# Optimization experiments

Hardware: AMD Instinct MI355X
Metric: run time of the kernel (lower is better)

The kernel has to match this reference:

```python
import jax, jax.numpy as jnp
import numpy as np

H = 64           # hidden_dim
ITERS = 24       # iterations
B, NV, NC, K = 16, 400, 440, 12   # graphs, vars/graph, clauses/graph, literals/clause
NPG = 2 * NV + NC                 # nodes per graph (2*NV literals then NC clauses)
N = B * NPG                       # total nodes = 19840


def setup_inputs() -> dict:
    rng = np.random.RandomState(0)
    key = jax.random.key(0)
    ks = iter(jax.random.split(key, 40))

    # mask: 0 for literal nodes, 1 for clause nodes
    mask_g = np.concatenate([np.zeros(2 * NV), np.ones(NC)]).astype(np.float32)
    mask = jnp.asarray(np.tile(mask_g, B))

    # flip permutation: per graph swap positive/negative literal halves, clauses identity
    perm_g = np.concatenate([np.arange(NV, 2 * NV), np.arange(NV), np.arange(2 * NV, NPG)])
    flip_perm = jnp.asarray((perm_g[None, :] + (np.arange(B) * NPG)[:, None]).ravel().astype(np.int32))

    # bipartite literal<->clause edges, both directions; self-loops added in reference
    off = (np.arange(B) * NPG)[:, None, None]
    lits = rng.randint(0, 2 * NV, size=(B, NC, K)) + off
    cls = np.broadcast_to((np.arange(NC) + 2 * NV)[None, :, None] + off, (B, NC, K))
    src = np.concatenate([lits.ravel(), cls.ravel()])
    dst = np.concatenate([cls.ravel(), lits.ravel()])
    edge_index = jnp.asarray(np.stack([src, dst]).astype(np.int32))

    def lin(i, o):
        return jax.random.normal(next(ks), (i, o), jnp.float32) / np.sqrt(i)

    def bias(o):
        return jax.random.normal(next(ks), (o,), jnp.float32) * 0.01

    x = jax.random.normal(next(ks), (N, 2), jnp.float32)
    return dict(
        x=x, mask=mask, edge_index=edge_index, flip_perm=flip_perm,
        li_w=lin(2, H), li_b=bias(H), ci_w=lin(2, H), ci_b=bias(H),
        lm1_w=lin(H, H), lm1_b=bias(H), lm2_w=lin(H, H), lm2_b=bias(H), lm3_w=lin(H, H), lm3_b=bias(H),
        cm1_w=lin(H, H), cm1_b=bias(H), cm2_w=lin(H, H), cm2_b=bias(H), cm3_w=lin(H, H), cm3_b=bias(H),
        lu_wih=lin(2 * H, 4 * H), lu_whh=lin(H, 4 * H), lu_bih=bias(4 * H), lu_bhh=bias(4 * H),
        cu_wih=lin(H, 4 * H), cu_whh=lin(H, 4 * H), cu_bih=bias(4 * H), cu_bhh=bias(4 * H),
        lv1_w=lin(H, H), lv1_b=bias(H), lv2_w=lin(H, H), lv2_b=bias(H), lv3_w=lin(H, 1), lv3_b=bias(1),
    )


def _mlp(h, w1, b1, w2, b2, w3, b3):
    # original MLP is three chained Linear layers with NO nonlinearity
    return ((h @ w1 + b1) @ w2 + b2) @ w3 + b3


def _lstm_cell(inp, h, c, wih, whh, bih, bhh):
    g = inp @ wih + h @ whh + bih + bhh          # [N, 4H], torch gate order i,f,g,o
    i, f, gg, o = jnp.split(g, 4, axis=-1)
    c2 = jax.nn.sigmoid(f) * c + jax.nn.sigmoid(i) * jnp.tanh(gg)
    h2 = jax.nn.sigmoid(o) * jnp.tanh(c2)
    return h2, c2


def _forward(x, mask, edge_index, flip_perm, params):
    (li_w, li_b, ci_w, ci_b,
     lm1_w, lm1_b, lm2_w, lm2_b, lm3_w, lm3_b,
     cm1_w, cm1_b, cm2_w, cm2_b, cm3_w, cm3_b,
     lu_wih, lu_whh, lu_bih, lu_bhh,
     cu_wih, cu_whh, cu_bih, cu_bhh,
     lv1_w, lv1_b, lv2_w, lv2_b, lv3_w, lv3_b) = params

    n = x.shape[0]
    sl = jnp.arange(n, dtype=edge_index.dtype)   # add_self_loops
    src = jnp.concatenate([edge_index[0], sl])
    dst = jnp.concatenate([edge_index[1], sl])
    m = mask[:, None]                            # [N,1]

    def prop(msgs):  # scatter-add aggregation: out[i] = sum_{(j->i)} msgs[j]
        return jax.ops.segment_sum(msgs[src], dst, num_segments=n)

    out = (x @ li_w + li_b) * (1 - m) + (x @ ci_w + ci_b) * m
    z = jnp.zeros_like(out)

    def step(carry, _):
        out, ch, cc, lh, lc = carry
        l_msg = prop(_mlp(out, lm1_w, lm1_b, lm2_w, lm2_b, lm3_w, lm3_b))
        ch, cc = _lstm_cell(l_msg, ch, cc, cu_wih, cu_whh, cu_bih, cu_bhh)
        temp = out * (1 - m) + ch * m
        c_msg = prop(_mlp(temp, cm1_w, cm1_b, cm2_w, cm2_b, cm3_w, cm3_b))
        c_in = jnp.concatenate([out[flip_perm], c_msg], axis=-1)  # flip via precomputed perm
        lh, lc = _lstm_cell(c_in, lh, lc, lu_wih, lu_whh, lu_bih, lu_bhh)
        out = lh * (1 - m) + ch * m
        return (out, ch, cc, lh, lc), None

    (out, _, _, _, _), _ = jax.lax.scan(step, (out, z, z, z, z), None, length=ITERS - 1)
    vote = _mlp(out * (1 - m), lv1_w, lv1_b, lv2_w, lv2_b, lv3_w, lv3_b)  # [N,1]
    return vote * (1 - m)


def reference(x, mask, edge_index, flip_perm,
              li_w, li_b, ci_w, ci_b,
              lm1_w, lm1_b, lm2_w, lm2_b, lm3_w, lm3_b,
              cm1_w, cm1_b, cm2_w, cm2_b, cm3_w, cm3_b,
              lu_wih, lu_whh, lu_bih, lu_bhh,
              cu_wih, cu_whh, cu_bih, cu_bhh,
              lv1_w, lv1_b, lv2_w, lv2_b, lv3_w, lv3_b):
    params = (li_w, li_b, ci_w, ci_b,
              lm1_w, lm1_b, lm2_w, lm2_b, lm3_w, lm3_b,
              cm1_w, cm1_b, cm2_w, cm2_b, cm3_w, cm3_b,
              lu_wih, lu_whh, lu_bih, lu_bhh,
              cu_wih, cu_whh, cu_bih, cu_bhh,
              lv1_w, lv1_b, lv2_w, lv2_b, lv3_w, lv3_b)
    return _forward(x, mask, edge_index, flip_perm, params)
```

## Files before the change

### kernel.cpp

```cpp
#include <hip/hip_runtime.h>
#include <math.h>


#define NV2_   800
#define NC_    440
#define KK_    12
#define NPG_   1240
#define NLIT_  12800
#define NCLS_  7040
#define NE_    84480
#define NN_    19840
#define STEPS_ 23

__device__ __forceinline__ float sigmf(float x) { return 1.0f / (1.0f + __expf(-x)); }
__device__ __forceinline__ float tanhf_(float x) { return 1.0f - 2.0f / (__expf(2.0f * x) + 1.0f); }


__global__ __launch_bounds__(64) void collapseT_k(
    const float* lm1, const float* lm1b, const float* lm2, const float* lm2b,
    const float* cm1, const float* cm1b, const float* cm2, const float* cm2b,
    float* T, float* ub)
{
    int r = blockIdx.x >> 6, i = blockIdx.x & 63, j = threadIdx.x;
    const float* w1 = r ? cm1 : lm1; const float* b1 = r ? cm1b : lm1b;
    const float* w2 = r ? cm2 : lm2; const float* b2 = r ? cm2b : lm2b;
    float s = 0.f;
    for (int k = 0; k < 64; ++k) s += w1[i * 64 + k] * w2[k * 64 + j];
    T[r * 4096 + i * 64 + j] = s;
    if (i == 0) {
        float s2 = 0.f;
        for (int k = 0; k < 64; ++k) s2 += b1[k] * w2[k * 64 + j];
        ub[r * 64 + j] = s2 + b2[j];
    }
}

__global__ __launch_bounds__(64) void collapseW_k(
    const float* lm3, const float* lm3b, const float* cm3, const float* cm3b,
    const float* T, const float* ub,
    float* Wl, float* bl, float* Wc, float* bc,
    const float* lv1, const float* lv1b, const float* lv2, const float* lv2b,
    const float* lv3, const float* lv3b, float* Wv, float* bv)
{
    int t = threadIdx.x;
    if (blockIdx.x < 128) {
        int r = blockIdx.x >> 6, i = blockIdx.x & 63, j = t;
        const float* w3 = r ? cm3 : lm3; const float* b3 = r ? cm3b : lm3b;
        float* W = r ? Wc : Wl; float* bb = r ? bc : bl;
        float s = 0.f;
        for (int k = 0; k < 64; ++k) s += T[r * 4096 + i * 64 + k] * w3[k * 64 + j];
        W[i * 64 + j] = s;
        if (i == 0) {
            float s2 = 0.f;
            for (int k = 0; k < 64; ++k) s2 += ub[r * 64 + k] * w3[k * 64 + j];
            bb[j] = s2 + b3[j];
        }
    } else {
        __shared__ float t3[64];
        __shared__ float ub2[64];
        float s = 0.f;
        for (int j = 0; j < 64; ++j) s += lv2[t * 64 + j] * lv3[j];
        t3[t] = s;
        float s2 = 0.f;
        for (int k = 0; k < 64; ++k) s2 += lv1b[k] * lv2[k * 64 + t];
        ub2[t] = s2 + lv2b[t];
        __syncthreads();
        float s3 = 0.f;
        for (int k = 0; k < 64; ++k) s3 += lv1[t * 64 + k] * t3[k];
        Wv[t] = s3;
        if (t == 0) {
            float v = 0.f;
            for (int j = 0; j < 64; ++j) v += ub2[j] * lv3[j];
            bv[0] = v + lv3b[0];
        }
    }
}

__global__ __launch_bounds__(256) void fold2_k(
    const float* Wl, const float* bl, const float* Wc, const float* bc,
    const float* lwih, const float* lbih, const float* lbhh,
    const float* cwih, const float* cbih, const float* cbhh,
    float* Wfl, float* bfl, float* Bl, float* Wfc, float* Bc)
{
    int t = blockIdx.x >> 6, i = blockIdx.x & 63, j = threadIdx.x;
    if (t == 0) {
        float s = 0.f;
        for (int m = 0; m < 64; ++m) s += Wc[i * 64 + m] * lwih[(64 + m) * 256 + j];
        Wfl[i * 256 + j] = s;
        if (i == 0) {
            float s2 = 0.f;
            for (int m = 0; m < 64; ++m) s2 += bc[m] * lwih[(64 + m) * 256 + j];
            bfl[j] = s2;
            Bl[j] = lbih[j] + lbhh[j];
        }
    } else {
        float s = 0.f;
        for (int m = 0; m < 64; ++m) s += Wl[i * 64 + m] * cwih[m * 256 + j];
        Wfc[i * 256 + j] = s;
        if (i == 0) {
            float s2 = 0.f;
            for (int m = 0; m < 64; ++m) s2 += bl[m] * cwih[m * 256 + j];
            Bc[j] = cbih[j] + cbhh[j] + 13.f * s2;
        }
    }
}

struct WT5 { const float* src[5]; float* dst[5]; };
__global__ __launch_bounds__(1024) void wtransAll_k(WT5 a)
{
    int m = blockIdx.x >> 4;
    int hc = blockIdx.x & 15;
    int half = hc >> 3, chunk = hc & 7;
    int t = threadIdx.x;
    int k = t >> 4, u4 = (t >> 2) & 3, g = t & 3;
    a.dst[m][(hc * 64 + k) * 16 + u4 * 4 + g] =
        a.src[m][k * 256 + g * 64 + half * 32 + chunk * 4 + u4];
}

__global__ __launch_bounds__(256) void init_k(
    const float* x, const float* liw, const float* lib, const float* ciw, const float* cib,
    float* out0, float* outc, float* chA, float* chB)
{
    int t = blockIdx.x * 256 + threadIdx.x;
    if (t < 64) {
        chA[(size_t)NCLS_ * 64 + t] = 0.f;
        chB[(size_t)NCLS_ * 64 + t] = 0.f;
    }
    if (t >= NN_ * 64) return;
    int node = t >> 6, j = t & 63;
    int b = node / NPG_;
    int i = node - b * NPG_;
    float x0 = x[node * 2 + 0], x1 = x[node * 2 + 1];
    if (i < NV2_) {
        int sp = (i < 400) ? 2 * i : 2 * (i - 400) + 1;
        out0[(size_t)(b * NV2_ + sp) * 64 + j] = x0 * liw[j] + x1 * liw[64 + j] + lib[j];
    } else {
        outc[(size_t)(b * NC_ + (i - NV2_)) * 64 + j] = x0 * ciw[j] + x1 * ciw[64 + j] + cib[j];
    }
}

__global__ __launch_bounds__(256) void econv_k(const int* ei, int* llits, int* cnt)
{
    int e = blockIdx.x * 256 + threadIdx.x;
    if (e >= NE_) return;
    int g = ei[e];
    int b = g / NPG_;
    int i = g - b * NPG_;
    int sp = (i < 400) ? 2 * i : 2 * (i - 400) + 1;
    int L = b * NV2_ + sp;
    llits[e] = L;
    atomicAdd(cnt + L, 1);
}

__global__ __launch_bounds__(1024) void scan_k(const int* cnt, int* rowptr, int* cursor)
{
    __shared__ int sums[1024];
    int t = threadIdx.x;
    int i0 = t * 13;
    int i1 = i0 + 13; if (i1 > NLIT_) i1 = NLIT_; if (i0 > NLIT_) i0 = NLIT_;
    int s = 0;
    for (int i = i0; i < i1; ++i) s += (cnt[i] + 7) & ~7;
    sums[t] = s;
    __syncthreads();
    for (int off = 1; off < 1024; off <<= 1) {
        int v = (t >= off) ? sums[t - off] : 0;
        __syncthreads();
        sums[t] += v;
        __syncthreads();
    }
    int run = sums[t] - s;
    for (int i = i0; i < i1; ++i) {
        rowptr[i] = run; cursor[i] = run;
        run += (cnt[i] + 7) & ~7;
    }
    if (t == 1023) rowptr[NLIT_] = sums[1023];
}

__global__ __launch_bounds__(256) void fill_k(const int* llits, int* cursor, int* col)
{
    int e = blockIdx.x * 256 + threadIdx.x;
    if (e >= NE_) return;
    int pos = atomicAdd(cursor + llits[e], 1);
    col[pos] = e / KK_;
}

__global__ __launch_bounds__(256) void pad_k(const int* cnt, const int* rowptr, int* col)
{
    int i = blockIdx.x * 256 + threadIdx.x;
    if (i >= NLIT_) return;
    for (int e = rowptr[i] + cnt[i]; e < rowptr[i + 1]; ++e) col[e] = NCLS_;
}


#define FMA16(rv, a,b,c,d) \
    acc[0]  = fmaf(rv, a.x, acc[0]);  acc[1]  = fmaf(rv, a.y, acc[1]);  \
    acc[2]  = fmaf(rv, a.z, acc[2]);  acc[3]  = fmaf(rv, a.w, acc[3]);  \
    acc[4]  = fmaf(rv, b.x, acc[4]);  acc[5]  = fmaf(rv, b.y, acc[5]);  \
    acc[6]  = fmaf(rv, b.z, acc[6]);  acc[7]  = fmaf(rv, b.w, acc[7]);  \
    acc[8]  = fmaf(rv, c.x, acc[8]);  acc[9]  = fmaf(rv, c.y, acc[9]);  \
    acc[10] = fmaf(rv, c.z, acc[10]); acc[11] = fmaf(rv, c.w, acc[11]); \
    acc[12] = fmaf(rv, d.x, acc[12]); acc[13] = fmaf(rv, d.y, acc[13]); \
    acc[14] = fmaf(rv, d.z, acc[14]); acc[15] = fmaf(rv, d.w, acc[15]);

__device__ __forceinline__ void gemmV(const float* __restrict__ Ls, int rx,
                                      const float* __restrict__ wb, float* acc)
{
    const int r = (threadIdx.x & 63) ^ rx;
    const float4* __restrict__ wp = (const float4*)wb;
#pragma unroll 4
    for (int k = 0; k < 64; ++k) {
        float4 w0 = wp[k * 4 + 0];
        float4 w1 = wp[k * 4 + 1];
        float4 w2 = wp[k * 4 + 2];
        float4 w3 = wp[k * 4 + 3];
        float rf = Ls[k * 65 + r];
        FMA16(rf, w0, w1, w2, w3);
    }
}

__device__ __forceinline__ void cellu(const float* a, float* c, float* h)
{
    float iv = sigmf(a[0]);
    float fv = sigmf(a[1]);
    float gv = tanhf_(a[2]);
    float ov = sigmf(a[3]);
    float c2 = fv * (*c) + iv * gv;
    *c = c2;
    *h = ov * tanhf_(c2);
}


__global__ __launch_bounds__(512, 4) void clause_step_k(
    const float* __restrict__ out_cur, const float* __restrict__ outc0,
    float* __restrict__ ch_cur, const float* __restrict__ ch_prev, float* __restrict__ ccg,
    const int* __restrict__ llits,
    const float* __restrict__ wfcT, const float* __restrict__ cwhhT,
    const float* __restrict__ Bc, int step)
{
    __shared__ float bufT[65 * 64];
    __shared__ float chT[65 * 64];
    const int tid = threadIdx.x;
    const int lane = tid & 63;
    const int wv = tid >> 6;
    const int half = blockIdx.x & 1;
    const int Cb = (blockIdx.x >> 1) * 64;
    const int chunk = __builtin_amdgcn_readfirstlane(wv);
    const int hc = half * 8 + chunk;

    for (int i = 0; i < 8; ++i) {
        int srow = wv * 8 + i;
        int c = Cb + srow;
        float v;
        if (step) {
            float ch0 = ch_prev[(size_t)c * 64 + lane];
            chT[lane * 65 + srow] = ch0;
            v = ch0;
        } else {
            v = outc0[(size_t)c * 64 + lane];
        }
        const int* lp = llits + c * KK_;
        float t0 = out_cur[(size_t)lp[0] * 64 + lane];
        float t1 = out_cur[(size_t)lp[1] * 64 + lane];
        float t2 = out_cur[(size_t)lp[2] * 64 + lane];
        float t3 = out_cur[(size_t)lp[3] * 64 + lane];
        float t4 = out_cur[(size_t)lp[4] * 64 + lane];
        float t5 = out_cur[(size_t)lp[5] * 64 + lane];
        float t6 = out_cur[(size_t)lp[6] * 64 + lane];
        float t7 = out_cur[(size_t)lp[7] * 64 + lane];
        float t8 = out_cur[(size_t)lp[8] * 64 + lane];
        float t9 = out_cur[(size_t)lp[9] * 64 + lane];
        float ta = out_cur[(size_t)lp[10] * 64 + lane];
        float tb = out_cur[(size_t)lp[11] * 64 + lane];
        v += t0 + t1 + t2 + t3 + t4 + t5 + t6 + t7 + t8 + t9 + ta + tb;
        bufT[lane * 65 + srow] = v;
    }
    __syncthreads();

    float acc[16];
    if (step) {
#pragma unroll
        for (int i = 0; i < 16; ++i) acc[i] = 0.f;
        gemmV(chT, 0, cwhhT + hc * 1024, acc);
#pragma unroll
        for (int u4 = 0; u4 < 4; ++u4)
#pragma unroll
            for (int g = 0; g < 4; ++g)
                acc[u4 * 4 + g] += Bc[g * 64 + half * 32 + chunk * 4 + u4];
    } else {
#pragma unroll
        for (int u4 = 0; u4 < 4; ++u4)
#pragma unroll
            for (int g = 0; g < 4; ++g)
                acc[u4 * 4 + g] = Bc[g * 64 + half * 32 + chunk * 4 + u4];
    }
    gemmV(bufT, 0, wfcT + hc * 1024, acc);

    const size_t rowbase = (size_t)(Cb + lane) * 64 + half * 32 + chunk * 4;
    float cc4[4], h4[4];
    if (step) {
        float4 cp = *(const float4*)(ccg + rowbase);
        cc4[0] = cp.x; cc4[1] = cp.y; cc4[2] = cp.z; cc4[3] = cp.w;
    } else { cc4[0] = cc4[1] = cc4[2] = cc4[3] = 0.f; }
#pragma unroll
    for (int u4 = 0; u4 < 4; ++u4) cellu(acc + u4 * 4, &cc4[u4], &h4[u4]);

    __syncthreads();
#pragma unroll
    for (int u4 = 0; u4 < 4; ++u4) {
        chT[lane * 33 + chunk * 4 + u4]  = h4[u4];
        bufT[lane * 33 + chunk * 4 + u4] = cc4[u4];
    }
    __syncthreads();
    {
        int row = tid >> 5, cl = tid & 31;
#pragma unroll
        for (int p = 0; p < 4; ++p) {
            int rr = row + p * 16;
            size_t dst = (size_t)(Cb + rr) * 64 + half * 32 + cl;
            ch_cur[dst] = chT[rr * 33 + cl];
            ccg[dst]    = bufT[rr * 33 + cl];
        }
    }
}

__global__ __launch_bounds__(512, 4) void lit_step_k(
    const float* __restrict__ out_cur, float* __restrict__ out_nxt,
    const float* __restrict__ chg, float* __restrict__ lcg,
    const int* __restrict__ rowptr, const int* __restrict__ col, const int* __restrict__ cnt,
    const float* __restrict__ wihT, const float* __restrict__ whhT, const float* __restrict__ wflT,
    const float* __restrict__ bfl, const float* __restrict__ Bl,
    const float* __restrict__ Wv, const float* __restrict__ bv, float* __restrict__ vout,
    int step)
{
    __shared__ float bufT[65 * 64 + 1024];
    const int tid = threadIdx.x;
    const int lane = tid & 63;
    const int wv = tid >> 6;
    const int half = blockIdx.x & 1;
    const int Lb = (blockIdx.x >> 1) * 64;
    const int chunk = __builtin_amdgcn_readfirstlane(wv);
    const int hc = half * 8 + chunk;

    for (int i = 0; i < 8; ++i) {
        int srow = wv * 8 + i;
        bufT[lane * 65 + srow] = out_cur[(size_t)(Lb + srow) * 64 + lane];
    }
    __syncthreads();

    const float degf = 1.f + (float)cnt[Lb + lane];
    float acc[16];
#pragma unroll
    for (int u4 = 0; u4 < 4; ++u4)
#pragma unroll
        for (int g = 0; g < 4; ++g) {
            int gc = g * 64 + half * 32 + chunk * 4 + u4;
            acc[u4 * 4 + g] = Bl[gc] + degf * bfl[gc];
        }
    gemmV(bufT, 1, wihT + hc * 1024, acc);
    if (step) gemmV(bufT, 0, whhT + hc * 1024, acc);
    __syncthreads();

    for (int i = 0; i < 8; ++i) {
        int srow = wv * 8 + i;
        int l = Lb + srow;
        int e = rowptr[l], eE = rowptr[l + 1];
        float v = bufT[lane * 65 + srow];
        for (; e < eE; e += 8) {
            float t0 = chg[(size_t)col[e    ] * 64 + lane];
            float t1 = chg[(size_t)col[e + 1] * 64 + lane];
            float t2 = chg[(size_t)col[e + 2] * 64 + lane];
            float t3 = chg[(size_t)col[e + 3] * 64 + lane];
            float t4 = chg[(size_t)col[e + 4] * 64 + lane];
            float t5 = chg[(size_t)col[e + 5] * 64 + lane];
            float t6 = chg[(size_t)col[e + 6] * 64 + lane];
            float t7 = chg[(size_t)col[e + 7] * 64 + lane];
            v += ((t0 + t1) + (t2 + t3)) + ((t4 + t5) + (t6 + t7));
        }
        bufT[lane * 65 + srow] = v;
    }
    __syncthreads();
    gemmV(bufT, 0, wflT + hc * 1024, acc);

    const size_t rowbase = (size_t)(Lb + lane) * 64 + half * 32 + chunk * 4;
    float lc4[4], h4[4];
    if (step) {
        float4 cp = *(const float4*)(lcg + rowbase);
        lc4[0] = cp.x; lc4[1] = cp.y; lc4[2] = cp.z; lc4[3] = cp.w;
    } else { lc4[0] = lc4[1] = lc4[2] = lc4[3] = 0.f; }
#pragma unroll
    for (int u4 = 0; u4 < 4; ++u4) cellu(acc + u4 * 4, &lc4[u4], &h4[u4]);

    float* hS = bufT;
    float* cS = bufT + 64 * 33;
    __syncthreads();
#pragma unroll
    for (int u4 = 0; u4 < 4; ++u4) {
        hS[lane * 33 + chunk * 4 + u4] = h4[u4];
        cS[lane * 33 + chunk * 4 + u4] = lc4[u4];
    }
    if (step == STEPS_ - 1) {
        float p = 0.f;
#pragma unroll
        for (int u4 = 0; u4 < 4; ++u4)
            p += h4[u4] * Wv[half * 32 + chunk * 4 + u4];
        bufT[64 * 66 + lane * 9 + chunk] = p;
    }
    __syncthreads();
    {
        int row = tid >> 5, cl = tid & 31;
#pragma unroll
        for (int p = 0; p < 4; ++p) {
            int rr = row + p * 16;
            size_t dst = (size_t)(Lb + rr) * 64 + half * 32 + cl;
            out_nxt[dst] = hS[rr * 33 + cl];
            lcg[dst]     = cS[rr * 33 + cl];
        }
    }
    if (step == STEPS_ - 1 && wv == 0) {
        float v = (half == 0) ? bv[0] : 0.f;
#pragma unroll
        for (int q = 0; q < 8; ++q) v += bufT[64 * 66 + lane * 9 + q];
        int R = Lb + lane;
        int b = R / NV2_;
        int pos = R - b * NV2_;
        int pi = (pos >> 1) + (pos & 1) * 400;
        atomicAdd(vout + b * NPG_ + pi, v);
    }
}


extern "C" void kernel_launch(void* const* d_in, const int* in_sizes, int n_in,
                              void* d_out, int out_size, void* d_ws, size_t ws_size,
                              hipStream_t stream)
{
    (void)in_sizes; (void)n_in; (void)out_size; (void)ws_size;
    const float* x    = (const float*)d_in[0];
    const int*   ei   = (const int*)d_in[2];
    const float* liw  = (const float*)d_in[4];
    const float* lib  = (const float*)d_in[5];
    const float* ciw  = (const float*)d_in[6];
    const float* cib  = (const float*)d_in[7];
    const float* lm1  = (const float*)d_in[8];
    const float* lm1b = (const float*)d_in[9];
    const float* lm2  = (const float*)d_in[10];
    const float* lm2b = (const float*)d_in[11];
    const float* lm3  = (const float*)d_in[12];
    const float* lm3b = (const float*)d_in[13];
    const float* cm1  = (const float*)d_in[14];
    const float* cm1b = (const float*)d_in[15];
    const float* cm2  = (const float*)d_in[16];
    const float* cm2b = (const float*)d_in[17];
    const float* cm3  = (const float*)d_in[18];
    const float* cm3b = (const float*)d_in[19];
    const float* lu_wih = (const float*)d_in[20];
    const float* lu_whh = (const float*)d_in[21];
    const float* lu_bih = (const float*)d_in[22];
    const float* lu_bhh = (const float*)d_in[23];
    const float* cu_wih = (const float*)d_in[24];
    const float* cu_whh = (const float*)d_in[25];
    const float* cu_bih = (const float*)d_in[26];
    const float* cu_bhh = (const float*)d_in[27];
    const float* lv1  = (const float*)d_in[28];
    const float* lv1b = (const float*)d_in[29];
    const float* lv2  = (const float*)d_in[30];
    const float* lv2b = (const float*)d_in[31];
    const float* lv3  = (const float*)d_in[32];
    const float* lv3b = (const float*)d_in[33];

    float* F = (float*)d_ws;
    size_t o = 0;
    auto A = [&](size_t n) { float* p = F + o; o += n; return p; };
    float* outA  = A((size_t)NLIT_ * 64);
    float* outB  = A((size_t)NLIT_ * 64);
    float* outc0 = A((size_t)NCLS_ * 64);
    float* chA   = A((size_t)(NCLS_ + 1) * 64);
    float* chB   = A((size_t)(NCLS_ + 1) * 64);
    float* ccg   = A((size_t)NCLS_ * 64);
    float* lcg   = A((size_t)NLIT_ * 64);
    float* Wl    = A(4096);
    float* Wc    = A(4096);
    float* bl    = A(64);
    float* bc    = A(64);
    float* Wv    = A(64);
    float* bv    = A(16);
    float* Wfl   = A(64 * 256);
    float* bfl   = A(256);
    float* Bl    = A(256);
    float* Wfc   = A(64 * 256);
    float* Bc    = A(256);
    float* Tbuf  = A(2 * 4096);
    float* ubuf  = A(2 * 64);
    float* wihT  = A(16384);
    float* whhT  = A(16384);
    float* wflT  = A(16384);
    float* cwhhT = A(16384);
    float* wfcT  = A(16384);
    int* I = (int*)(F + o);
    int* llits  = I; I += NE_;
    int* rowptr = I; I += 12804;
    int* cursor = I; I += NLIT_;
    int* pcol   = I; I += 184320;
    int* cnt    = I; I += NLIT_;

    hipMemsetAsync(cnt, 0, NLIT_ * sizeof(int), stream);
    hipMemsetAsync(d_out, 0, (size_t)NN_ * sizeof(float), stream);

    collapseT_k<<<128, 64, 0, stream>>>(lm1, lm1b, lm2, lm2b, cm1, cm1b, cm2, cm2b, Tbuf, ubuf);
    collapseW_k<<<129, 64, 0, stream>>>(lm3, lm3b, cm3, cm3b, Tbuf, ubuf, Wl, bl, Wc, bc,
                                        lv1, lv1b, lv2, lv2b, lv3, lv3b, Wv, bv);
    fold2_k<<<128, 256, 0, stream>>>(Wl, bl, Wc, bc,
                                     lu_wih, lu_bih, lu_bhh,
                                     cu_wih, cu_bih, cu_bhh,
                                     Wfl, bfl, Bl, Wfc, Bc);
    WT5 wt;
    wt.src[0] = lu_wih; wt.dst[0] = wihT;
    wt.src[1] = lu_whh; wt.dst[1] = whhT;
    wt.src[2] = Wfl;    wt.dst[2] = wflT;
    wt.src[3] = cu_whh; wt.dst[3] = cwhhT;
    wt.src[4] = Wfc;    wt.dst[4] = wfcT;
    wtransAll_k<<<80, 1024, 0, stream>>>(wt);
    init_k<<<(NN_ * 64 + 255) / 256, 256, 0, stream>>>(x, liw, lib, ciw, cib,
                                                       outA, outc0, chA, chB);
    econv_k<<<NE_ / 256, 256, 0, stream>>>(ei, llits, cnt);
    scan_k<<<1, 1024, 0, stream>>>(cnt, rowptr, cursor);
    fill_k<<<NE_ / 256, 256, 0, stream>>>(llits, cursor, pcol);
    pad_k<<<(NLIT_ + 255) / 256, 256, 0, stream>>>(cnt, rowptr, pcol);

    for (int s = 0; s < STEPS_; ++s) {
        const float* oc  = (s & 1) ? outB : outA;
        float*       on  = (s & 1) ? outA : outB;
        float*       chc = (s & 1) ? chA : chB;
        const float* chp = (s & 1) ? chB : chA;
        clause_step_k<<<220, 512, 0, stream>>>(oc, outc0, chc, chp, ccg,
                                               llits, wfcT, cwhhT, Bc, s);
        lit_step_k<<<400, 512, 0, stream>>>(oc, on, chc, lcg, rowptr, pcol, cnt,
                                            wihT, whhT, wflT, bfl, Bl,
                                            Wv, bv, (float*)d_out, s);
    }
}
```

Measured before the change: 1.344 ms.

## Process 128 rows per block so each weight load feeds two row accumulators

The clause and literal step kernels now handle 128 nodes per block instead of 64. Each thread keeps two sets of 16 accumulators, so every float4 weight fetched in the inner GEMM loop is reused for two rows. The write-back is also switched to float4 stores. This halves the weight traffic per node, but it also halves the grid (110 and 200 blocks on a large GPU), lowers occupancy through launch bounds and larger LDS use, and raises register pressure.

```diff
diff --git a/kernel.cpp b/kernel.cpp
--- a/kernel.cpp
+++ b/kernel.cpp
@@ -11,6 +11,7 @@
 #define NE_    84480
 #define NN_    19840
 #define STEPS_ 23
+#define LSTR_  129
 
 __device__ __forceinline__ float sigmf(float x) { return 1.0f / (1.0f + __expf(-x)); }
 __device__ __forceinline__ float tanhf_(float x) { return 1.0f - 2.0f / (__expf(2.0f * x) + 1.0f); }
@@ -191,7 +192,7 @@
 }
 
 
-#define FMA16(rv, a,b,c,d) \
+#define FMA16P(rv, a,b,c,d, acc) \
     acc[0]  = fmaf(rv, a.x, acc[0]);  acc[1]  = fmaf(rv, a.y, acc[1]);  \
     acc[2]  = fmaf(rv, a.z, acc[2]);  acc[3]  = fmaf(rv, a.w, acc[3]);  \
     acc[4]  = fmaf(rv, b.x, acc[4]);  acc[5]  = fmaf(rv, b.y, acc[5]);  \
@@ -201,10 +202,10 @@
     acc[12] = fmaf(rv, d.x, acc[12]); acc[13] = fmaf(rv, d.y, acc[13]); \
     acc[14] = fmaf(rv, d.z, acc[14]); acc[15] = fmaf(rv, d.w, acc[15]);
 
-__device__ __forceinline__ void gemmV(const float* __restrict__ Ls, int rx,
-                                      const float* __restrict__ wb, float* acc)
-{
-    const int r = (threadIdx.x & 63) ^ rx;
+__device__ __forceinline__ void gemmD(const float* __restrict__ Ls, int rA, int rB,
+                                      const float* __restrict__ wb,
+                                      float* accA, float* accB)
+{
     const float4* __restrict__ wp = (const float4*)wb;
 #pragma unroll 4
     for (int k = 0; k < 64; ++k) {
@@ -212,8 +213,10 @@
         float4 w1 = wp[k * 4 + 1];
         float4 w2 = wp[k * 4 + 2];
         float4 w3 = wp[k * 4 + 3];
-        float rf = Ls[k * 65 + r];
-        FMA16(rf, w0, w1, w2, w3);
+        float fA = Ls[k * LSTR_ + rA];
+        float fB = Ls[k * LSTR_ + rB];
+        FMA16P(fA, w0, w1, w2, w3, accA);
+        FMA16P(fB, w0, w1, w2, w3, accB);
     }
 }
 
@@ -229,30 +232,30 @@
 }
 
 
-__global__ __launch_bounds__(512, 4) void clause_step_k(
+__global__ __launch_bounds__(512, 2) void clause_step_k(
     const float* __restrict__ out_cur, const float* __restrict__ outc0,
     float* __restrict__ ch_cur, const float* __restrict__ ch_prev, float* __restrict__ ccg,
     const int* __restrict__ llits,
     const float* __restrict__ wfcT, const float* __restrict__ cwhhT,
     const float* __restrict__ Bc, int step)
 {
-    __shared__ float bufT[65 * 64];
-    __shared__ float chT[65 * 64];
+    __shared__ float bufT[64 * LSTR_ + 192];
+    __shared__ float chT[64 * LSTR_ + 192];
     const int tid = threadIdx.x;
     const int lane = tid & 63;
     const int wv = tid >> 6;
     const int half = blockIdx.x & 1;
-    const int Cb = (blockIdx.x >> 1) * 64;
+    const int Cb = (blockIdx.x >> 1) * 128;
     const int chunk = __builtin_amdgcn_readfirstlane(wv);
     const int hc = half * 8 + chunk;
 
-    for (int i = 0; i < 8; ++i) {
-        int srow = wv * 8 + i;
+    for (int i = 0; i < 16; ++i) {
+        int srow = wv * 16 + i;
         int c = Cb + srow;
         float v;
         if (step) {
             float ch0 = ch_prev[(size_t)c * 64 + lane];
-            chT[lane * 65 + srow] = ch0;
+            chT[lane * LSTR_ + srow] = ch0;
             v = ch0;
         } else {
             v = outc0[(size_t)c * 64 + lane];
@@ -271,58 +274,77 @@
         float ta = out_cur[(size_t)lp[10] * 64 + lane];
         float tb = out_cur[(size_t)lp[11] * 64 + lane];
         v += t0 + t1 + t2 + t3 + t4 + t5 + t6 + t7 + t8 + t9 + ta + tb;
-        bufT[lane * 65 + srow] = v;
-    }
-    __syncthreads();
-
-    float acc[16];
+        bufT[lane * LSTR_ + srow] = v;
+    }
+    __syncthreads();
+
+    const int rA = lane, rB = lane + 64;
+    float accA[16], accB[16];
     if (step) {
-#pragma unroll
-        for (int i = 0; i < 16; ++i) acc[i] = 0.f;
-        gemmV(chT, 0, cwhhT + hc * 1024, acc);
+        float wA[16], wB[16];
+#pragma unroll
+        for (int i = 0; i < 16; ++i) { wA[i] = 0.f; wB[i] = 0.f; }
+        gemmD(chT, rA, rB, cwhhT + hc * 1024, wA, wB);
 #pragma unroll
         for (int u4 = 0; u4 < 4; ++u4)
 #pragma unroll
-            for (int g = 0; g < 4; ++g)
-                acc[u4 * 4 + g] += Bc[g * 64 + half * 32 + chunk * 4 + u4];
+            for (int g = 0; g < 4; ++g) {
+                float b = Bc[g * 64 + half * 32 + chunk * 4 + u4];
+                accA[u4 * 4 + g] = b + wA[u4 * 4 + g];
+                accB[u4 * 4 + g] = b + wB[u4 * 4 + g];
+            }
     } else {
 #pragma unroll
         for (int u4 = 0; u4 < 4; ++u4)
 #pragma unroll
-            for (int g = 0; g < 4; ++g)
-                acc[u4 * 4 + g] = Bc[g * 64 + half * 32 + chunk * 4 + u4];
-    }
-    gemmV(bufT, 0, wfcT + hc * 1024, acc);
-
-    const size_t rowbase = (size_t)(Cb + lane) * 64 + half * 32 + chunk * 4;
-    float cc4[4], h4[4];
+            for (int g = 0; g < 4; ++g) {
+                float b = Bc[g * 64 + half * 32 + chunk * 4 + u4];
+                accA[u4 * 4 + g] = b;
+                accB[u4 * 4 + g] = b;
+            }
+    }
+    gemmD(bufT, rA, rB, wfcT + hc * 1024, accA, accB);
+
+    const size_t baseA = (size_t)(Cb + rA) * 64 + half * 32 + chunk * 4;
+    const size_t baseB = (size_t)(Cb + rB) * 64 + half * 32 + chunk * 4;
+    float ccA[4], ccB[4], hA[4], hB[4];
     if (step) {
-        float4 cp = *(const float4*)(ccg + rowbase);
-        cc4[0] = cp.x; cc4[1] = cp.y; cc4[2] = cp.z; cc4[3] = cp.w;
-    } else { cc4[0] = cc4[1] = cc4[2] = cc4[3] = 0.f; }
-#pragma unroll
-    for (int u4 = 0; u4 < 4; ++u4) cellu(acc + u4 * 4, &cc4[u4], &h4[u4]);
-
-    __syncthreads();
+        float4 pa = *(const float4*)(ccg + baseA);
+        float4 pb = *(const float4*)(ccg + baseB);
+        ccA[0] = pa.x; ccA[1] = pa.y; ccA[2] = pa.z; ccA[3] = pa.w;
+        ccB[0] = pb.x; ccB[1] = pb.y; ccB[2] = pb.z; ccB[3] = pb.w;
+    } else {
+#pragma unroll
+        for (int q = 0; q < 4; ++q) { ccA[q] = 0.f; ccB[q] = 0.f; }
+    }
 #pragma unroll
     for (int u4 = 0; u4 < 4; ++u4) {
-        chT[lane * 33 + chunk * 4 + u4]  = h4[u4];
-        bufT[lane * 33 + chunk * 4 + u4] = cc4[u4];
+        cellu(accA + u4 * 4, &ccA[u4], &hA[u4]);
+        cellu(accB + u4 * 4, &ccB[u4], &hB[u4]);
+    }
+
+    __syncthreads();
+    float* hS = chT;
+    float* cS = bufT;
+#pragma unroll
+    for (int u4 = 0; u4 < 4; ++u4) {
+        hS[rA * 33 + chunk * 4 + u4] = hA[u4];
+        hS[rB * 33 + chunk * 4 + u4] = hB[u4];
+        cS[rA * 33 + chunk * 4 + u4] = ccA[u4];
+        cS[rB * 33 + chunk * 4 + u4] = ccB[u4];
     }
     __syncthreads();
     {
-        int row = tid >> 5, cl = tid & 31;
-#pragma unroll
-        for (int p = 0; p < 4; ++p) {
-            int rr = row + p * 16;
-            size_t dst = (size_t)(Cb + rr) * 64 + half * 32 + cl;
-            ch_cur[dst] = chT[rr * 33 + cl];
-            ccg[dst]    = bufT[rr * 33 + cl];
-        }
-    }
-}
-
-__global__ __launch_bounds__(512, 4) void lit_step_k(
+        int row = tid >> 2, c8 = (tid & 3) << 3;
+        size_t dst = (size_t)(Cb + row) * 64 + half * 32 + c8;
+        *(float4*)(ch_cur + dst)     = *(float4*)(hS + row * 33 + c8);
+        *(float4*)(ch_cur + dst + 4) = *(float4*)(hS + row * 33 + c8 + 4);
+        *(float4*)(ccg + dst)        = *(float4*)(cS + row * 33 + c8);
+        *(float4*)(ccg + dst + 4)    = *(float4*)(cS + row * 33 + c8 + 4);
+    }
+}
+
+__global__ __launch_bounds__(512, 2) void lit_step_k(
     const float* __restrict__ out_cur, float* __restrict__ out_nxt,
     const float* __restrict__ chg, float* __restrict__ lcg,
     const int* __restrict__ rowptr, const int* __restrict__ col, const int* __restrict__ cnt,
@@ -331,39 +353,45 @@
     const float* __restrict__ Wv, const float* __restrict__ bv, float* __restrict__ vout,
     int step)
 {
-    __shared__ float bufT[65 * 64 + 1024];
+    __shared__ float bufT[64 * LSTR_ + 192];
+    __shared__ float st2[128 * 33 + 64];
+    __shared__ float pv[128 * 9];
     const int tid = threadIdx.x;
     const int lane = tid & 63;
     const int wv = tid >> 6;
     const int half = blockIdx.x & 1;
-    const int Lb = (blockIdx.x >> 1) * 64;
+    const int Lb = (blockIdx.x >> 1) * 128;
     const int chunk = __builtin_amdgcn_readfirstlane(wv);
     const int hc = half * 8 + chunk;
 
-    for (int i = 0; i < 8; ++i) {
-        int srow = wv * 8 + i;
-        bufT[lane * 65 + srow] = out_cur[(size_t)(Lb + srow) * 64 + lane];
-    }
-    __syncthreads();
-
-    const float degf = 1.f + (float)cnt[Lb + lane];
-    float acc[16];
+    for (int i = 0; i < 16; ++i) {
+        int srow = wv * 16 + i;
+        bufT[lane * LSTR_ + srow] = out_cur[(size_t)(Lb + srow) * 64 + lane];
+    }
+    __syncthreads();
+
+    const int rA = lane, rB = lane + 64;
+    const float degA = 1.f + (float)cnt[Lb + rA];
+    const float degB = 1.f + (float)cnt[Lb + rB];
+    float accA[16], accB[16];
 #pragma unroll
     for (int u4 = 0; u4 < 4; ++u4)
 #pragma unroll
         for (int g = 0; g < 4; ++g) {
             int gc = g * 64 + half * 32 + chunk * 4 + u4;
-            acc[u4 * 4 + g] = Bl[gc] + degf * bfl[gc];
-        }
-    gemmV(bufT, 1, wihT + hc * 1024, acc);
-    if (step) gemmV(bufT, 0, whhT + hc * 1024, acc);
-    __syncthreads();
-
-    for (int i = 0; i < 8; ++i) {
-        int srow = wv * 8 + i;
+            float b = Bl[gc], f = bfl[gc];
+            accA[u4 * 4 + g] = b + degA * f;
+            accB[u4 * 4 + g] = b + degB * f;
+        }
+    gemmD(bufT, rA ^ 1, rB ^ 1, wihT + hc * 1024, accA, accB);
+    if (step) gemmD(bufT, rA, rB, whhT + hc * 1024, accA, accB);
+    __syncthreads();
+
+    for (int i = 0; i < 16; ++i) {
+        int srow = wv * 16 + i;
         int l = Lb + srow;
         int e = rowptr[l], eE = rowptr[l + 1];
-        float v = bufT[lane * 65 + srow];
+        float v = bufT[lane * LSTR_ + srow];
         for (; e < eE; e += 8) {
             float t0 = chg[(size_t)col[e    ] * 64 + lane];
             float t1 = chg[(size_t)col[e + 1] * 64 + lane];
@@ -375,55 +403,72 @@
             float t7 = chg[(size_t)col[e + 7] * 64 + lane];
             v += ((t0 + t1) + (t2 + t3)) + ((t4 + t5) + (t6 + t7));
         }
-        bufT[lane * 65 + srow] = v;
-    }
-    __syncthreads();
-    gemmV(bufT, 0, wflT + hc * 1024, acc);
-
-    const size_t rowbase = (size_t)(Lb + lane) * 64 + half * 32 + chunk * 4;
-    float lc4[4], h4[4];
+        bufT[lane * LSTR_ + srow] = v;
+    }
+    __syncthreads();
+    gemmD(bufT, rA, rB, wflT + hc * 1024, accA, accB);
+
+    const size_t baseA = (size_t)(Lb + rA) * 64 + half * 32 + chunk * 4;
+    const size_t baseB = (size_t)(Lb + rB) * 64 + half * 32 + chunk * 4;
+    float lcA[4], lcB[4], hA[4], hB[4];
     if (step) {
-        float4 cp = *(const float4*)(lcg + rowbase);
-        lc4[0] = cp.x; lc4[1] = cp.y; lc4[2] = cp.z; lc4[3] = cp.w;
-    } else { lc4[0] = lc4[1] = lc4[2] = lc4[3] = 0.f; }
-#pragma unroll
-    for (int u4 = 0; u4 < 4; ++u4) cellu(acc + u4 * 4, &lc4[u4], &h4[u4]);
-
+        float4 pa = *(const float4*)(lcg + baseA);
+        float4 pb = *(const float4*)(lcg + baseB);
+        lcA[0] = pa.x; lcA[1] = pa.y; lcA[2] = pa.z; lcA[3] = pa.w;
+        lcB[0] = pb.x; lcB[1] = pb.y; lcB[2] = pb.z; lcB[3] = pb.w;
+    } else {
+#pragma unroll
+        for (int q = 0; q < 4; ++q) { lcA[q] = 0.f; lcB[q] = 0.f; }
+    }
+#pragma unroll
+    for (int u4 = 0; u4 < 4; ++u4) {
+        cellu(accA + u4 * 4, &lcA[u4], &hA[u4]);
+        cellu(accB + u4 * 4, &lcB[u4], &hB[u4]);
+    }
+
+    __syncthreads();
     float* hS = bufT;
-    float* cS = bufT + 64 * 33;
-    __syncthreads();
+    float* cS = st2;
 #pragma unroll
     for (int u4 = 0; u4 < 4; ++u4) {
-        hS[lane * 33 + chunk * 4 + u4] = h4[u4];
-        cS[lane * 33 + chunk * 4 + u4] = lc4[u4];
+        hS[rA * 33 + chunk * 4 + u4] = hA[u4];
+        hS[rB * 33 + chunk * 4 + u4] = hB[u4];
+        cS[rA * 33 + chunk * 4 + u4] = lcA[u4];
+        cS[rB * 33 + chunk * 4 + u4] = lcB[u4];
     }
     if (step == STEPS_ - 1) {
-        float p = 0.f;
-#pragma unroll
-        for (int u4 = 0; u4 < 4; ++u4)
-            p += h4[u4] * Wv[half * 32 + chunk * 4 + u4];
-        bufT[64 * 66 + lane * 9 + chunk] = p;
+        float pA = 0.f, pB = 0.f;
+#pragma unroll
+        for (int u4 = 0; u4 < 4; ++u4) {
+            float w = Wv[half * 32 + chunk * 4 + u4];
+            pA += hA[u4] * w;
+            pB += hB[u4] * w;
+        }
+        pv[rA * 9 + chunk] = pA;
+        pv[rB * 9 + chunk] = pB;
     }
     __syncthreads();
     {
-        int row = tid >> 5, cl = tid & 31;
-#pragma unroll
-        for (int p = 0; p < 4; ++p) {
-            int rr = row + p * 16;
-            size_t dst = (size_t)(Lb + rr) * 64 + half * 32 + cl;
-            out_nxt[dst] = hS[rr * 33 + cl];
-            lcg[dst]     = cS[rr * 33 + cl];
-        }
+        int row = tid >> 2, c8 = (tid & 3) << 3;
+        size_t dst = (size_t)(Lb + row) * 64 + half * 32 + c8;
+        *(float4*)(out_nxt + dst)     = *(float4*)(hS + row * 33 + c8);
+        *(float4*)(out_nxt + dst + 4) = *(float4*)(hS + row * 33 + c8 + 4);
+        *(float4*)(lcg + dst)         = *(float4*)(cS + row * 33 + c8);
+        *(float4*)(lcg + dst + 4)     = *(float4*)(cS + row * 33 + c8 + 4);
     }
     if (step == STEPS_ - 1 && wv == 0) {
-        float v = (half == 0) ? bv[0] : 0.f;
-#pragma unroll
-        for (int q = 0; q < 8; ++q) v += bufT[64 * 66 + lane * 9 + q];
-        int R = Lb + lane;
-        int b = R / NV2_;
-        int pos = R - b * NV2_;
-        int pi = (pos >> 1) + (pos & 1) * 400;
-        atomicAdd(vout + b * NPG_ + pi, v);
+#pragma unroll
+        for (int rr = 0; rr < 2; ++rr) {
+            int row = lane + rr * 64;
+            float v = (half == 0) ? bv[0] : 0.f;
+#pragma unroll
+            for (int q = 0; q < 8; ++q) v += pv[row * 9 + q];
+            int R = Lb + row;
+            int b = R / NV2_;
+            int pos = R - b * NV2_;
+            int pi = (pos >> 1) + (pos & 1) * 400;
+            atomicAdd(vout + b * NPG_ + pi, v);
+        }
     }
 }
 
@@ -530,9 +575,9 @@
         float*       on  = (s & 1) ? outA : outB;
         float*       chc = (s & 1) ? chA : chB;
         const float* chp = (s & 1) ? chB : chA;
-        clause_step_k<<<220, 512, 0, stream>>>(oc, outc0, chc, chp, ccg,
+        clause_step_k<<<110, 512, 0, stream>>>(oc, outc0, chc, chp, ccg,
                                                llits, wfcT, cwhhT, Bc, s);
-        lit_step_k<<<400, 512, 0, stream>>>(oc, on, chc, lcg, rowptr, pcol, cnt,
+        lit_step_k<<<200, 512, 0, stream>>>(oc, on, chc, lcg, rowptr, pcol, cnt,
                                             wihT, whhT, wflT, bfl, Bl,
                                             Wv, bv, (float*)d_out, s);
     }
```

Result: slower. 1.852 ms (+37.7%).
